# Optimization experiments

Hardware: AMD Instinct MI355X
Metric: run time of the kernel (lower is better)

## Reference

```python
import jax, jax.numpy as jnp
import numpy as np

B, NQ, NK, DIM, H = 2, 2048, 4096, 256, 8
HD = DIM // H  # head dim = 32


def setup_inputs() -> dict:
    key = jax.random.key(0)
    ks = jax.random.split(key, 8)
    s = 0.02  # init scale for weights
    return {
        "xq": jax.random.normal(ks[0], (B, NQ, DIM), jnp.float32),
        "xk": jax.random.normal(ks[1], (B, NK, DIM), jnp.float32),
        "xv": jax.random.normal(ks[2], (B, NK, DIM), jnp.float32),
        # torch nn.Linear weights: shape (out, in), y = x @ W.T + b
        "wq": jax.random.normal(ks[3], (DIM, DIM), jnp.float32) * s,
        "wk": jax.random.normal(ks[4], (DIM, DIM), jnp.float32) * s,
        "wv": jax.random.normal(ks[5], (DIM, DIM), jnp.float32) * s,
        "wp": jax.random.normal(ks[6], (DIM, DIM), jnp.float32) * s,
        "bp": jnp.zeros((DIM,), jnp.float32),
    }


def reference(xq, xk, xv, wq, wk, wv, wp, bp):
    scale = HD ** (-0.5)
    Bq, Nq, C = xq.shape
    Nk = xk.shape[1]
    # project and split heads: [B, H, N, HD]
    q = jnp.einsum('bnc,dc->bnd', xq, wq).reshape(Bq, Nq, H, HD).transpose(0, 2, 1, 3)
    k = jnp.einsum('bnc,dc->bnd', xk, wk).reshape(Bq, Nk, H, HD).transpose(0, 2, 1, 3)
    v = jnp.einsum('bnc,dc->bnd', xv, wv).reshape(Bq, Nk, H, HD).transpose(0, 2, 1, 3)
    # pre-softmax scores [B, H, Nq, Nk]
    attn = jnp.einsum('bhqd,bhkd->bhqk', q, k) * scale
    attn_save = attn.sum(axis=1) / H  # head-mean of pre-softmax scores
    p = jax.nn.softmax(attn, axis=-1)
    x = jnp.einsum('bhqk,bhkd->bhqd', p, v).transpose(0, 2, 1, 3).reshape(Bq, Nq, C)
    x = jnp.einsum('bnc,dc->bnd', x, wp) + bp
    return x, attn_save
```

## Files before the change

### kernel.cpp

```cpp
#include <hip/hip_runtime.h>

typedef unsigned int u32;
typedef unsigned short u16;
typedef short bf16x8 __attribute__((ext_vector_type(8)));
typedef float f32x4 __attribute__((ext_vector_type(4)));
typedef float f32x16 __attribute__((ext_vector_type(16)));
typedef int i32x4 __attribute__((ext_vector_type(4)));
typedef __bf16 bf16x2 __attribute__((ext_vector_type(2)));
typedef float f32x2 __attribute__((ext_vector_type(2)));

#define KSPLIT 4

__device__ __forceinline__ u32 pack2bf(float a, float b) {
    u32 ua = __float_as_uint(a), ub = __float_as_uint(b);
    ua = (ua + 0x7fffu + ((ua >> 16) & 1u)) >> 16;
    ub = (ub + 0x7fffu + ((ub >> 16) & 1u)) >> 16;
    return (ua & 0xffffu) | (ub << 16);
}
__device__ __forceinline__ u16 bf1(float a) {
    u32 ua = __float_as_uint(a);
    return (u16)((ua + 0x7fffu + ((ua >> 16) & 1u)) >> 16);
}
__device__ __forceinline__ u32 b2(float a, float b) {
    f32x2 f; f[0] = a; f[1] = b;
    bf16x2 h = __builtin_convertvector(f, bf16x2);
    return __builtin_bit_cast(u32, h);
}

__global__ __launch_bounds__(256) void cvt_w4(const float* __restrict__ wq,
                                              const float* __restrict__ wk,
                                              const float* __restrict__ wv,
                                              const float* __restrict__ wp,
                                              u16* __restrict__ dst) {
    int i = blockIdx.x * 256 + threadIdx.x;
    int which = i >> 14;
    int j = i & 16383;
    const float* s = which == 0 ? wq : which == 1 ? wk : which == 2 ? wv : wp;
    float4 a = ((const float4*)s)[j];
    uint2 v;
    v.x = pack2bf(a.x, a.y);
    v.y = pack2bf(a.z, a.w);
    ((uint2*)(dst + which * 65536))[j] = v;
}

__global__ __launch_bounds__(256) void proj_all(const float* __restrict__ xq,
                                                const float* __restrict__ xk,
                                                const float* __restrict__ xv,
                                                const u16* __restrict__ W4,
                                                u16* __restrict__ Qb,
                                                u16* __restrict__ K2,
                                                u16* __restrict__ V2,
                                                float qalpha) {
    int bx = blockIdx.x;
    int mode = bx < 64 ? 0 : (bx < 192 ? 1 : 2);
    int xb = mode == 0 ? bx : (mode == 1 ? bx - 64 : bx - 192);
    const float* X = mode == 0 ? xq : mode == 1 ? xk : xv;
    const u16* Wb = W4 + mode * 65536;

    __shared__ u16 xs[64 * 256];
    int t = threadIdx.x;
    int m0 = xb * 64;
#pragma unroll
    for (int i = 0; i < 8; i++) {
        int c16 = t + 256 * i;
        int row = c16 >> 5, col16 = c16 & 31;
        const float4* src = (const float4*)(X + (size_t)(m0 + row) * 256 + col16 * 8);
        float4 a = src[0], b2v = src[1];
        uint4 v;
        v.x = pack2bf(a.x, a.y); v.y = pack2bf(a.z, a.w);
        v.z = pack2bf(b2v.x, b2v.y); v.w = pack2bf(b2v.z, b2v.w);
        int byteoff = row * 512 + ((col16 * 16) ^ ((row & 7) << 4));
        *(uint4*)((char*)xs + byteoff) = v;
    }
    __syncthreads();
    int lane = t & 63, w = t >> 6;
    int lq = lane & 15, g = lane >> 4;
    int rowA = w * 16 + lq;
    f32x4 acc[16];
    f32x4 z = {0.f, 0.f, 0.f, 0.f};
#pragma unroll
    for (int nt = 0; nt < 16; nt++) acc[nt] = z;
#pragma unroll
    for (int kk = 0; kk < 8; kk++) {
        bf16x8 aF = *(const bf16x8*)((const char*)xs + rowA * 512 +
                                     ((kk * 64 + g * 16) ^ ((rowA & 7) << 4)));
#pragma unroll
        for (int nt = 0; nt < 16; nt++) {
            bf16x8 bF = *(const bf16x8*)(Wb + (size_t)(nt * 16 + lq) * 256 + kk * 32 + g * 8);
            acc[nt] = __builtin_amdgcn_mfma_f32_16x16x32_bf16(aF, bF, acc[nt], 0, 0, 0);
        }
    }
    if (mode == 0) {
#pragma unroll
        for (int nt = 0; nt < 16; nt++) {
            int col = nt * 16 + lq;
#pragma unroll
            for (int r = 0; r < 4; r++) {
                int m = m0 + w * 16 + g * 4 + r;
                Qb[(size_t)m * 256 + col] = bf1(acc[nt][r] * qalpha);
            }
        }
    } else if (mode == 1) {
        int m = m0 + w * 16 + g * 4;
        int b = m >> 12, n = m & 4095;
#pragma unroll
        for (int nt = 0; nt < 16; nt++) {
            int d = nt * 16 + lq;
            int h = d >> 5, d32 = d & 31;
            u16* p = K2 + ((size_t)(b * 8 + h) * 4096 + n) * 32 + d32;
#pragma unroll
            for (int r = 0; r < 4; r++) p[r * 32] = bf1(acc[nt][r]);
        }
    } else {
        int m = m0 + w * 16 + g * 4;
        int b = m >> 12, n = m & 4095;
        int s = n >> 5;
        int t5 = n & 31;
        int pklo = (t5 & 19) | ((t5 << 1) & 8) | ((t5 >> 1) & 4);
#pragma unroll
        for (int nt = 0; nt < 16; nt++) {
            int d = nt * 16 + lq;
            int h = d >> 5, d32 = d & 31;
            uint2 v;
            v.x = pack2bf(acc[nt][0], acc[nt][1]);
            v.y = pack2bf(acc[nt][2], acc[nt][3]);
            *(uint2*)(V2 + ((((size_t)(b * 8 + h) * 128 + s) * 32 + d32) * 32 + pklo)) = v;
        }
    }
}

__global__ __launch_bounds__(256) void save_gemm(const u16* __restrict__ Qb,
                                                 const u16* __restrict__ K2,
                                                 float* __restrict__ sv) {
    const float SAVE = 0.125f * 0.69314718055994530942f;
    int b = blockIdx.z;
    int m0 = blockIdx.y * 128, n0 = blockIdx.x * 128;
    int t = threadIdx.x, lane = t & 63, wv = t >> 6;
    int wr = wv >> 1, wc = wv & 1;
    int lq = lane & 15, g = lane >> 4;
    const u16* Q = Qb + (size_t)b * 2048 * 256;
    f32x4 acc[4][4];
    f32x4 z = {0.f, 0.f, 0.f, 0.f};
#pragma unroll
    for (int mt = 0; mt < 4; mt++)
#pragma unroll
        for (int nt = 0; nt < 4; nt++) acc[mt][nt] = z;
#pragma unroll
    for (int kk = 0; kk < 8; kk++) {
        bf16x8 aF[4], bF[4];
#pragma unroll
        for (int mt = 0; mt < 4; mt++)
            aF[mt] = *(const bf16x8*)(Q + (size_t)(m0 + wr * 64 + mt * 16 + lq) * 256 + kk * 32 + g * 8);
#pragma unroll
        for (int nt = 0; nt < 4; nt++)
            bF[nt] = *(const bf16x8*)(K2 + ((size_t)(b * 8 + kk) * 4096 + n0 + wc * 64 + nt * 16 + lq) * 32 + g * 8);
#pragma unroll
        for (int mt = 0; mt < 4; mt++)
#pragma unroll
            for (int nt = 0; nt < 4; nt++)
                acc[mt][nt] = __builtin_amdgcn_mfma_f32_16x16x32_bf16(aF[mt], bF[nt], acc[mt][nt], 0, 0, 0);
    }
#pragma unroll
    for (int mt = 0; mt < 4; mt++) {
#pragma unroll
        for (int nt = 0; nt < 4; nt++) {
            int col = n0 + wc * 64 + nt * 16 + lq;
#pragma unroll
            for (int r = 0; r < 4; r++) {
                int row = m0 + wr * 64 + mt * 16 + g * 4 + r;
                sv[((size_t)b * 2048 + row) * 4096 + col] = acc[mt][nt][r] * SAVE;
            }
        }
    }
}

__global__ __launch_bounds__(256, 2) void attn_part(const u16* __restrict__ Qb,
                                                    const u16* __restrict__ K2,
                                                    const u16* __restrict__ V2,
                                                    float* __restrict__ PO,
                                                    float* __restrict__ PL) {
    int id = blockIdx.x;
    int h = id & 7;
    int r0 = id >> 3;
    int qblk = r0 & 7;
    int b = (r0 >> 3) & 1;
    int part = r0 >> 4;
    int bh = b * 8 + h;
    int t = threadIdx.x, lane = t & 63, w = t >> 6;
    int lq = lane & 31, hl = lane >> 5;
    int qa = qblk * 256 + w * 64 + lq;
    const u16* Qrow = Qb + ((size_t)(b * 2048 + qa)) * 256 + h * 32 + hl * 8;
    bf16x8 qf00 = *(const bf16x8*)(Qrow);
    bf16x8 qf01 = *(const bf16x8*)(Qrow + 16);
    bf16x8 qf10 = *(const bf16x8*)(Qrow + 32 * 256);
    bf16x8 qf11 = *(const bf16x8*)(Qrow + 32 * 256 + 16);
    const u16* Kh = K2 + ((size_t)bh * 4096 + part * 1024 + lq) * 32 + hl * 8;
    const u16* Vh = V2 + (size_t)bh * 131072 + part * 32768 + lq * 32 + hl * 8;
    f32x16 z16 = {};
    f32x16 o0 = z16, o1 = z16;
    float l0 = 0.f, l1 = 0.f;
    for (int it = 0; it < 16; ++it) {
#pragma unroll
        for (int s = 0; s < 2; s++) {
            const u16* kp = Kh + (it * 64 + s * 32) * 32;
            bf16x8 kf0 = *(const bf16x8*)(kp);
            bf16x8 kf1 = *(const bf16x8*)(kp + 16);
            const u16* vp = Vh + (it * 2 + s) * 1024;
            bf16x8 vf0 = *(const bf16x8*)(vp);
            bf16x8 vf1 = *(const bf16x8*)(vp + 16);
            f32x16 sA = __builtin_amdgcn_mfma_f32_32x32x16_bf16(kf0, qf00, z16, 0, 0, 0);
            sA = __builtin_amdgcn_mfma_f32_32x32x16_bf16(kf1, qf01, sA, 0, 0, 0);
            f32x16 sB = __builtin_amdgcn_mfma_f32_32x32x16_bf16(kf0, qf10, z16, 0, 0, 0);
            sB = __builtin_amdgcn_mfma_f32_32x32x16_bf16(kf1, qf11, sB, 0, 0, 0);
            float pA[16], pB[16];
#pragma unroll
            for (int k = 0; k < 16; k++) pA[k] = __builtin_amdgcn_exp2f(sA[k]);
#pragma unroll
            for (int k = 0; k < 16; k++) pB[k] = __builtin_amdgcn_exp2f(sB[k]);
            float la = 0.f, lb = 0.f;
#pragma unroll
            for (int k = 0; k < 16; k++) { la += pA[k]; lb += pB[k]; }
            l0 += la; l1 += lb;
            i32x4 wa0, wa1, wb0, wb1;
#pragma unroll
            for (int j = 0; j < 4; j++) {
                wa0[j] = (int)b2(pA[2 * j], pA[2 * j + 1]);
                wa1[j] = (int)b2(pA[8 + 2 * j], pA[9 + 2 * j]);
                wb0[j] = (int)b2(pB[2 * j], pB[2 * j + 1]);
                wb1[j] = (int)b2(pB[8 + 2 * j], pB[9 + 2 * j]);
            }
            bf16x8 pa0 = __builtin_bit_cast(bf16x8, wa0);
            bf16x8 pa1 = __builtin_bit_cast(bf16x8, wa1);
            bf16x8 pb0 = __builtin_bit_cast(bf16x8, wb0);
            bf16x8 pb1 = __builtin_bit_cast(bf16x8, wb1);
            o0 = __builtin_amdgcn_mfma_f32_32x32x16_bf16(vf0, pa0, o0, 0, 0, 0);
            o0 = __builtin_amdgcn_mfma_f32_32x32x16_bf16(vf1, pa1, o0, 0, 0, 0);
            o1 = __builtin_amdgcn_mfma_f32_32x32x16_bf16(vf0, pb0, o1, 0, 0, 0);
            o1 = __builtin_amdgcn_mfma_f32_32x32x16_bf16(vf1, pb1, o1, 0, 0, 0);
        }
    }
    l0 += __shfl_xor(l0, 32);
    l1 += __shfl_xor(l1, 32);
    size_t rowa = (size_t)(part * 16 + bh) * 2048 + qa;
    float* poa = PO + rowa * 32;
    float* pob = PO + (rowa + 32) * 32;
#pragma unroll
    for (int cc = 0; cc < 4; cc++) {
        f32x4 va, vb;
#pragma unroll
        for (int i = 0; i < 4; i++) { va[i] = o0[4 * cc + i]; vb[i] = o1[4 * cc + i]; }
        *(f32x4*)(poa + cc * 8 + hl * 4) = va;
        *(f32x4*)(pob + cc * 8 + hl * 4) = vb;
    }
    if (hl == 0) {
        PL[rowa] = l0;
        PL[rowa + 32] = l1;
    }
}

__global__ __launch_bounds__(256) void combine_oproj(const float* __restrict__ PO,
                                                     const float* __restrict__ PL,
                                                     const u16* __restrict__ Wp,
                                                     const float* __restrict__ bp,
                                                     float* __restrict__ out) {
    __shared__ u16 os[16 * 256];
    int t = threadIdx.x;
    int qloc = t >> 4, chunk = t & 15;
    int R = blockIdx.x * 16 + qloc;
    int b = R >> 11, q = R & 2047;
    int h = chunk >> 1;
    int d0 = chunk * 16;
    int d32 = d0 & 31;
    int bh = b * 8 + h;
    float acc[16];
#pragma unroll
    for (int j = 0; j < 16; j++) acc[j] = 0.f;
    float L = 0.f;
#pragma unroll
    for (int p = 0; p < KSPLIT; p++) {
        size_t i = ((size_t)(p * 16 + bh) << 11) + q;
        L += PL[i];
        const f32x4* src = (const f32x4*)(PO + i * 32 + d32);
#pragma unroll
        for (int v = 0; v < 4; v++) {
            f32x4 x = src[v];
#pragma unroll
            for (int e = 0; e < 4; e++) acc[4 * v + e] += x[e];
        }
    }
    float inv = 1.0f / L;
    uint4 w0, w1;
    w0.x = b2(acc[0] * inv, acc[1] * inv);   w0.y = b2(acc[2] * inv, acc[3] * inv);
    w0.z = b2(acc[4] * inv, acc[5] * inv);   w0.w = b2(acc[6] * inv, acc[7] * inv);
    w1.x = b2(acc[8] * inv, acc[9] * inv);   w1.y = b2(acc[10] * inv, acc[11] * inv);
    w1.z = b2(acc[12] * inv, acc[13] * inv); w1.w = b2(acc[14] * inv, acc[15] * inv);
    int col16a = d0 >> 3;
    *(uint4*)((char*)os + qloc * 512 + ((col16a * 16) ^ ((qloc & 7) << 4))) = w0;
    *(uint4*)((char*)os + qloc * 512 + (((col16a + 1) * 16) ^ ((qloc & 7) << 4))) = w1;
    __syncthreads();
    int lane = t & 63, w = t >> 6;
    int lq = lane & 15, g = lane >> 4;
    int nb = w * 4;
    f32x4 acc4[4];
    f32x4 z = {0.f, 0.f, 0.f, 0.f};
#pragma unroll
    for (int j = 0; j < 4; j++) acc4[j] = z;
#pragma unroll
    for (int kk = 0; kk < 8; kk++) {
        bf16x8 aF = *(const bf16x8*)((const char*)os + lq * 512 +
                                     ((kk * 64 + g * 16) ^ ((lq & 7) << 4)));
#pragma unroll
        for (int j = 0; j < 4; j++) {
            bf16x8 bF = *(const bf16x8*)(Wp + (size_t)((nb + j) * 16 + lq) * 256 + kk * 32 + g * 8);
            acc4[j] = __builtin_amdgcn_mfma_f32_16x16x32_bf16(aF, bF, acc4[j], 0, 0, 0);
        }
    }
    int R0 = blockIdx.x * 16;
#pragma unroll
    for (int j = 0; j < 4; j++) {
        int col = (nb + j) * 16 + lq;
        float bias = bp[col];
#pragma unroll
        for (int r = 0; r < 4; r++) {
            int row = R0 + g * 4 + r;
            out[(size_t)row * 256 + col] = acc4[j][r] + bias;
        }
    }
}

extern "C" void kernel_launch(void* const* d_in, const int* in_sizes, int n_in,
                              void* d_out, int out_size, void* d_ws, size_t ws_size,
                              hipStream_t stream) {
    const float* xq = (const float*)d_in[0];
    const float* xk = (const float*)d_in[1];
    const float* xv = (const float*)d_in[2];
    const float* wq = (const float*)d_in[3];
    const float* wk = (const float*)d_in[4];
    const float* wv = (const float*)d_in[5];
    const float* wp = (const float*)d_in[6];
    const float* bp = (const float*)d_in[7];
    float* out = (float*)d_out;

    u16* wsb = (u16*)d_ws;
    u16* W4 = wsb;
    u16* WPb = wsb + 196608;
    u16* Qb = wsb + 262144;
    u16* K2 = Qb + 1048576;
    u16* V2 = K2 + 2097152;

    float* outw = out + 1048576;
    float* PO = outw;
    float* PL = PO + 4194304;

    const float qalpha = 0.17677669529663687f * 1.4426950408889634f;

    cvt_w4<<<256, 256, 0, stream>>>(wq, wk, wv, wp, W4);
    proj_all<<<320, 256, 0, stream>>>(xq, xk, xv, W4, Qb, K2, V2, qalpha);

    attn_part<<<512, 256, 0, stream>>>(Qb, K2, V2, PO, PL);
    combine_oproj<<<256, 256, 0, stream>>>(PO, PL, WPb, bp, out);

    save_gemm<<<dim3(32, 16, 2), 256, 0, stream>>>(Qb, K2, out + 1048576);
}
```

Baseline: 113.1 us.

## Halve per-wave query rows in attention and store partial outputs as fp16

Each wave in the split-K attention kernel now handles 32 query rows instead of 64, and the grid doubles to 1024 blocks with an occupancy hint of 3. This spreads the work across more wavefronts and frees registers, at the cost of loading each K/V tile twice as often per query. Partial outputs are also written to scratch as fp16 rather than fp32 and widened in the combine kernel, which halves that intermediate traffic but adds some rounding error on the unnormalized partial sums.

```diff
diff --git a/kernel.cpp b/kernel.cpp
--- a/kernel.cpp
+++ b/kernel.cpp
@@ -4,10 +4,13 @@
 typedef unsigned short u16;
 typedef short bf16x8 __attribute__((ext_vector_type(8)));
 typedef float f32x4 __attribute__((ext_vector_type(4)));
+typedef float f32x8 __attribute__((ext_vector_type(8)));
 typedef float f32x16 __attribute__((ext_vector_type(16)));
 typedef int i32x4 __attribute__((ext_vector_type(4)));
 typedef __bf16 bf16x2 __attribute__((ext_vector_type(2)));
 typedef float f32x2 __attribute__((ext_vector_type(2)));
+typedef _Float16 f16x2t __attribute__((ext_vector_type(2)));
+typedef _Float16 f16x8 __attribute__((ext_vector_type(8)));
 
 #define KSPLIT 4
 
@@ -24,6 +27,11 @@
 __device__ __forceinline__ u32 b2(float a, float b) {
     f32x2 f; f[0] = a; f[1] = b;
     bf16x2 h = __builtin_convertvector(f, bf16x2);
+    return __builtin_bit_cast(u32, h);
+}
+__device__ __forceinline__ u32 h2(float a, float b) {
+    f32x2 f; f[0] = a; f[1] = b;
+    f16x2t h = __builtin_convertvector(f, f16x2t);
     return __builtin_bit_cast(u32, h);
 }
 
@@ -174,31 +182,29 @@
     }
 }
 
-__global__ __launch_bounds__(256, 2) void attn_part(const u16* __restrict__ Qb,
+__global__ __launch_bounds__(256, 3) void attn_part(const u16* __restrict__ Qb,
                                                     const u16* __restrict__ K2,
                                                     const u16* __restrict__ V2,
-                                                    float* __restrict__ PO,
+                                                    _Float16* __restrict__ PO,
                                                     float* __restrict__ PL) {
     int id = blockIdx.x;
     int h = id & 7;
     int r0 = id >> 3;
-    int qblk = r0 & 7;
-    int b = (r0 >> 3) & 1;
-    int part = r0 >> 4;
+    int qblk = r0 & 15;
+    int b = (r0 >> 4) & 1;
+    int part = r0 >> 5;
     int bh = b * 8 + h;
     int t = threadIdx.x, lane = t & 63, w = t >> 6;
     int lq = lane & 31, hl = lane >> 5;
-    int qa = qblk * 256 + w * 64 + lq;
+    int qa = qblk * 128 + w * 32 + lq;
     const u16* Qrow = Qb + ((size_t)(b * 2048 + qa)) * 256 + h * 32 + hl * 8;
-    bf16x8 qf00 = *(const bf16x8*)(Qrow);
-    bf16x8 qf01 = *(const bf16x8*)(Qrow + 16);
-    bf16x8 qf10 = *(const bf16x8*)(Qrow + 32 * 256);
-    bf16x8 qf11 = *(const bf16x8*)(Qrow + 32 * 256 + 16);
+    bf16x8 qf0 = *(const bf16x8*)(Qrow);
+    bf16x8 qf1 = *(const bf16x8*)(Qrow + 16);
     const u16* Kh = K2 + ((size_t)bh * 4096 + part * 1024 + lq) * 32 + hl * 8;
     const u16* Vh = V2 + (size_t)bh * 131072 + part * 32768 + lq * 32 + hl * 8;
     f32x16 z16 = {};
-    f32x16 o0 = z16, o1 = z16;
-    float l0 = 0.f, l1 = 0.f;
+    f32x16 o0 = z16;
+    float l0 = 0.f;
     for (int it = 0; it < 16; ++it) {
 #pragma unroll
         for (int s = 0; s < 2; s++) {
@@ -208,57 +214,41 @@
             const u16* vp = Vh + (it * 2 + s) * 1024;
             bf16x8 vf0 = *(const bf16x8*)(vp);
             bf16x8 vf1 = *(const bf16x8*)(vp + 16);
-            f32x16 sA = __builtin_amdgcn_mfma_f32_32x32x16_bf16(kf0, qf00, z16, 0, 0, 0);
-            sA = __builtin_amdgcn_mfma_f32_32x32x16_bf16(kf1, qf01, sA, 0, 0, 0);
-            f32x16 sB = __builtin_amdgcn_mfma_f32_32x32x16_bf16(kf0, qf10, z16, 0, 0, 0);
-            sB = __builtin_amdgcn_mfma_f32_32x32x16_bf16(kf1, qf11, sB, 0, 0, 0);
-            float pA[16], pB[16];
+            f32x16 sA = __builtin_amdgcn_mfma_f32_32x32x16_bf16(kf0, qf0, z16, 0, 0, 0);
+            sA = __builtin_amdgcn_mfma_f32_32x32x16_bf16(kf1, qf1, sA, 0, 0, 0);
+            float pA[16];
 #pragma unroll
             for (int k = 0; k < 16; k++) pA[k] = __builtin_amdgcn_exp2f(sA[k]);
-#pragma unroll
-            for (int k = 0; k < 16; k++) pB[k] = __builtin_amdgcn_exp2f(sB[k]);
-            float la = 0.f, lb = 0.f;
-#pragma unroll
-            for (int k = 0; k < 16; k++) { la += pA[k]; lb += pB[k]; }
-            l0 += la; l1 += lb;
-            i32x4 wa0, wa1, wb0, wb1;
+            float la = 0.f;
+#pragma unroll
+            for (int k = 0; k < 16; k++) la += pA[k];
+            l0 += la;
+            i32x4 wa0, wa1;
 #pragma unroll
             for (int j = 0; j < 4; j++) {
                 wa0[j] = (int)b2(pA[2 * j], pA[2 * j + 1]);
                 wa1[j] = (int)b2(pA[8 + 2 * j], pA[9 + 2 * j]);
-                wb0[j] = (int)b2(pB[2 * j], pB[2 * j + 1]);
-                wb1[j] = (int)b2(pB[8 + 2 * j], pB[9 + 2 * j]);
             }
             bf16x8 pa0 = __builtin_bit_cast(bf16x8, wa0);
             bf16x8 pa1 = __builtin_bit_cast(bf16x8, wa1);
-            bf16x8 pb0 = __builtin_bit_cast(bf16x8, wb0);
-            bf16x8 pb1 = __builtin_bit_cast(bf16x8, wb1);
             o0 = __builtin_amdgcn_mfma_f32_32x32x16_bf16(vf0, pa0, o0, 0, 0, 0);
             o0 = __builtin_amdgcn_mfma_f32_32x32x16_bf16(vf1, pa1, o0, 0, 0, 0);
-            o1 = __builtin_amdgcn_mfma_f32_32x32x16_bf16(vf0, pb0, o1, 0, 0, 0);
-            o1 = __builtin_amdgcn_mfma_f32_32x32x16_bf16(vf1, pb1, o1, 0, 0, 0);
         }
     }
     l0 += __shfl_xor(l0, 32);
-    l1 += __shfl_xor(l1, 32);
     size_t rowa = (size_t)(part * 16 + bh) * 2048 + qa;
-    float* poa = PO + rowa * 32;
-    float* pob = PO + (rowa + 32) * 32;
+    _Float16* poa = PO + rowa * 32;
 #pragma unroll
     for (int cc = 0; cc < 4; cc++) {
-        f32x4 va, vb;
-#pragma unroll
-        for (int i = 0; i < 4; i++) { va[i] = o0[4 * cc + i]; vb[i] = o1[4 * cc + i]; }
-        *(f32x4*)(poa + cc * 8 + hl * 4) = va;
-        *(f32x4*)(pob + cc * 8 + hl * 4) = vb;
-    }
-    if (hl == 0) {
-        PL[rowa] = l0;
-        PL[rowa + 32] = l1;
-    }
-}
-
-__global__ __launch_bounds__(256) void combine_oproj(const float* __restrict__ PO,
+        uint2 v;
+        v.x = h2(o0[4 * cc + 0], o0[4 * cc + 1]);
+        v.y = h2(o0[4 * cc + 2], o0[4 * cc + 3]);
+        *(uint2*)(poa + cc * 8 + hl * 4) = v;
+    }
+    if (hl == 0) PL[rowa] = l0;
+}
+
+__global__ __launch_bounds__(256) void combine_oproj(const _Float16* __restrict__ PO,
                                                      const float* __restrict__ PL,
                                                      const u16* __restrict__ Wp,
                                                      const float* __restrict__ bp,
@@ -280,13 +270,11 @@
     for (int p = 0; p < KSPLIT; p++) {
         size_t i = ((size_t)(p * 16 + bh) << 11) + q;
         L += PL[i];
-        const f32x4* src = (const f32x4*)(PO + i * 32 + d32);
-#pragma unroll
-        for (int v = 0; v < 4; v++) {
-            f32x4 x = src[v];
-#pragma unroll
-            for (int e = 0; e < 4; e++) acc[4 * v + e] += x[e];
-        }
+        const f16x8* src = (const f16x8*)(PO + i * 32 + d32);
+        f32x8 x0 = __builtin_convertvector(src[0], f32x8);
+        f32x8 x1 = __builtin_convertvector(src[1], f32x8);
+#pragma unroll
+        for (int e = 0; e < 8; e++) { acc[e] += x0[e]; acc[8 + e] += x1[e]; }
     }
     float inv = 1.0f / L;
     uint4 w0, w1;
@@ -349,15 +337,15 @@
     u16* V2 = K2 + 2097152;
 
     float* outw = out + 1048576;
-    float* PO = outw;
-    float* PL = PO + 4194304;
+    _Float16* PO = (_Float16*)outw;
+    float* PL = outw + 2097152;
 
     const float qalpha = 0.17677669529663687f * 1.4426950408889634f;
 
     cvt_w4<<<256, 256, 0, stream>>>(wq, wk, wv, wp, W4);
     proj_all<<<320, 256, 0, stream>>>(xq, xk, xv, W4, Qb, K2, V2, qalpha);
 
-    attn_part<<<512, 256, 0, stream>>>(Qb, K2, V2, PO, PL);
+    attn_part<<<1024, 256, 0, stream>>>(Qb, K2, V2, PO, PL);
     combine_oproj<<<256, 256, 0, stream>>>(PO, PL, WPb, bp, out);
 
     save_gemm<<<dim3(32, 16, 2), 256, 0, stream>>>(Qb, K2, out + 1048576);
```

Result: slower. 121.5 us (+7.4%).
